# Kernel optimization log

Measured on AMD Instinct MI355X. Metric: run time of the kernel, lower is better.

The kernel has to match this reference:

```python
import jax, jax.numpy as jnp
import numpy as np

N_NODES = 50000
N_EDGES = 640000
DIM_IN = 128
DIM_OUT = 32
HEADS = 4
NEG_SLOPE = 0.2


def setup_inputs() -> dict:
    key = jax.random.key(0)
    ks = jax.random.split(key, 8)
    HC = HEADS * DIM_OUT
    x = jax.random.normal(ks[0], (N_NODES, DIM_IN), dtype=jnp.float32)
    edge_index = jax.random.randint(ks[1], (2, N_EDGES), 0, N_NODES, dtype=jnp.int32)
    s = 1.0 / np.sqrt(DIM_IN)
    Wl = jax.random.normal(ks[2], (DIM_IN, HC), dtype=jnp.float32) * s   # lin_l (source)
    Wr = jax.random.normal(ks[3], (DIM_IN, HC), dtype=jnp.float32) * s   # lin_r (target)
    att = jax.random.normal(ks[4], (HEADS, DIM_OUT), dtype=jnp.float32) * (1.0 / np.sqrt(DIM_OUT))
    bias = jnp.zeros((HC,), dtype=jnp.float32)
    Wp = jax.random.normal(ks[5], (HC, DIM_OUT), dtype=jnp.float32) * (1.0 / np.sqrt(HC))
    bp = jnp.zeros((DIM_OUT,), dtype=jnp.float32)
    return {"x": x, "edge_index": edge_index, "Wl": Wl, "Wr": Wr,
            "att": att, "bias": bias, "Wp": Wp, "bp": bp}


def reference(x, edge_index, Wl, Wr, att, bias, Wp, bp):
    N = x.shape[0]
    H, C = att.shape
    src = edge_index[0]  # j: message source
    dst = edge_index[1]  # i: message target (softmax segment)
    xl = (x @ Wl).reshape(N, H, C)  # source-side transform
    xr = (x @ Wr).reshape(N, H, C)  # target-side transform
    # GATv2: e_ij = a^T LeakyReLU(xl_j + xr_i)
    e = jax.nn.leaky_relu(xl[src] + xr[dst], NEG_SLOPE)        # [E,H,C]
    logits = jnp.einsum('ehc,hc->eh', e, att)                  # [E,H]
    m = jax.ops.segment_max(logits, dst, num_segments=N)       # [N,H]
    ex = jnp.exp(logits - m[dst])
    denom = jax.ops.segment_sum(ex, dst, num_segments=N)       # [N,H]
    alpha = ex / (denom[dst] + 1e-16)                          # [E,H]
    msg = xl[src] * alpha[:, :, None]                          # [E,H,C]
    out = jax.ops.segment_sum(msg, dst, num_segments=N)        # [N,H,C]
    out = out.reshape(N, H * C) + bias                         # concat heads + bias
    return out @ Wp + bp                                       # proj to dim_out
```

## Files before the change

kernel.cpp:

```cpp
#include <hip/hip_runtime.h>
#include <hip/hip_bf16.h>
#include <math.h>

#define N_NODES 50000
#define N_EDGES 640000
#define HEADS 4
#define CDIM 32
#define HC 128
#define DIN 128
#define DOUT 32
#define NEG_SLOPE 0.2f
#define TPAD 136
#define BCAP 64
#define NPB 16
#define EPT 4
#define ZERO_NB ((N_NODES + 255) / 256)
#define WT_NB (2 * DIN * HC / 256)
#define WPT_NB (DOUT * HC / 256)
#define FILL_NB (N_EDGES / (256 * EPT))
#define TF_NB ((N_NODES + 127) / 128)

typedef __hip_bfloat16 bf16;
typedef __attribute__((ext_vector_type(8))) short short8;
typedef __attribute__((ext_vector_type(4))) float floatx4;
typedef __attribute__((ext_vector_type(2))) float floatx2;
typedef __attribute__((ext_vector_type(4))) unsigned short ushort4v;

static __device__ __forceinline__ float bflo(unsigned w) { return __uint_as_float(w << 16); }
static __device__ __forceinline__ float bfhi(unsigned w) { return __uint_as_float(w & 0xFFFF0000u); }
static __device__ __forceinline__ unsigned short f2bf(float f) {
    union { bf16 h; unsigned short u; } cv; cv.h = __float2bfloat16(f); return cv.u;
}

__global__ __launch_bounds__(256) void k_prep(
    unsigned* __restrict__ cnt,
    const float* __restrict__ Wl, const float* __restrict__ Wr,
    const float* __restrict__ bias, const float* __restrict__ Wp,
    const float* __restrict__ bp,
    bf16* __restrict__ WlF, bf16* __restrict__ WrF, bf16* __restrict__ WpT,
    float* __restrict__ cvec)
{
    const int t = threadIdx.x, b = blockIdx.x;
    if (b < ZERO_NB) {
        const int i = b * 256 + t;
        if (i < N_NODES) cnt[i] = 0u;
    } else if (b < ZERO_NB + WT_NB) {
        const int i = (b - ZERO_NB) * 256 + t;
        const int i2 = (i < DIN * HC) ? i : i - DIN * HC;
        const int c = i2 >> 7, j = i2 & 127;
        const int jt = j >> 4, m = j & 15;
        const int kk = c >> 5, quad = (c >> 3) & 3, u = c & 7;
        const int idx = (jt * 4 + kk) * 512 + (quad * 16 + m) * 8 + u;
        if (i < DIN * HC) WlF[idx] = __float2bfloat16(Wl[i2]);
        else              WrF[idx] = __float2bfloat16(Wr[i2]);
    } else if (b < ZERO_NB + WT_NB + WPT_NB) {
        const int i = (b - ZERO_NB - WT_NB) * 256 + t;
        const int c = i >> 5, j = i & 31;
        WpT[j * HC + c] = __float2bfloat16(Wp[i]);
    } else {
        __shared__ float part[8][32];
        const int j = t & 31, ch = t >> 5;
        float v = 0.f;
        for (int c = ch * 16; c < ch * 16 + 16; c++)
            v += bias[c] * Wp[c * DOUT + j];
        part[ch][j] = v;
        __syncthreads();
        if (t < 32) {
            float s = bp[t];
            #pragma unroll
            for (int k = 0; k < 8; k++) s += part[k][t];
            cvec[t] = s;
        }
    }
}

__global__ __launch_bounds__(256) void k_fill_tf(
    const int* __restrict__ ei, unsigned* __restrict__ cnt,
    unsigned short* __restrict__ srcs,
    const float* __restrict__ x,
    const bf16* __restrict__ WlF, const bf16* __restrict__ WrF,
    bf16* __restrict__ xl, bf16* __restrict__ xr)
{
    const int t = threadIdx.x, b = blockIdx.x;

    if (b < FILL_NB) {
        const int e0 = (b * 256 + t) * EPT;
        const int4 sv = *(const int4*)(ei + e0);
        const int4 dv = *(const int4*)(ei + N_EDGES + e0);
        const int s[4] = {sv.x, sv.y, sv.z, sv.w};
        const int d[4] = {dv.x, dv.y, dv.z, dv.w};
        unsigned pos[4];
        #pragma unroll
        for (int i = 0; i < EPT; i++)
            pos[i] = atomicAdd(&cnt[d[i]], 1u);
        #pragma unroll
        for (int i = 0; i < EPT; i++)
            if (pos[i] < BCAP)
                srcs[((size_t)d[i] << 6) + pos[i]] = (unsigned short)s[i];
        return;
    }

    const int n0 = (b - FILL_NB) * 128;
    const int w = t >> 6, lane = t & 63;
    const int m = lane & 15, quad = lane >> 4;
    const int na = n0 + w * 32 + m;
    const int nb = na + 16;
    const bool va = (na < N_NODES), vb = (nb < N_NODES);

    const float* xpa = x + (size_t)(va ? na : 0) * DIN;
    const float* xpb = x + (size_t)(vb ? nb : 0) * DIN;
    short8 afa[4], afb[4];
    #pragma unroll
    for (int kk = 0; kk < 4; kk++) {
        const float4 la = *(const float4*)(xpa + kk * 32 + quad * 8);
        const float4 ha = *(const float4*)(xpa + kk * 32 + quad * 8 + 4);
        const float4 lb = *(const float4*)(xpb + kk * 32 + quad * 8);
        const float4 hb = *(const float4*)(xpb + kk * 32 + quad * 8 + 4);
        short8 va8, vb8;
        va8[0] = (short)f2bf(la.x); va8[1] = (short)f2bf(la.y);
        va8[2] = (short)f2bf(la.z); va8[3] = (short)f2bf(la.w);
        va8[4] = (short)f2bf(ha.x); va8[5] = (short)f2bf(ha.y);
        va8[6] = (short)f2bf(ha.z); va8[7] = (short)f2bf(ha.w);
        vb8[0] = (short)f2bf(lb.x); vb8[1] = (short)f2bf(lb.y);
        vb8[2] = (short)f2bf(lb.z); vb8[3] = (short)f2bf(lb.w);
        vb8[4] = (short)f2bf(hb.x); vb8[5] = (short)f2bf(hb.y);
        vb8[6] = (short)f2bf(hb.z); vb8[7] = (short)f2bf(hb.w);
        afa[kk] = va8;
        afb[kk] = vb8;
    }

    const short8* wlf = (const short8*)WlF;
    const short8* wrf = (const short8*)WrF;
    #pragma unroll
    for (int jt = 0; jt < 8; jt++) {
        floatx4 aLa = {0.f,0.f,0.f,0.f}, aLb = {0.f,0.f,0.f,0.f};
        floatx4 aRa = {0.f,0.f,0.f,0.f}, aRb = {0.f,0.f,0.f,0.f};
        #pragma unroll
        for (int kk = 0; kk < 4; kk++) {
            const short8 bl = wlf[(jt * 4 + kk) * 64 + lane];
            const short8 br = wrf[(jt * 4 + kk) * 64 + lane];
            aLa = __builtin_amdgcn_mfma_f32_16x16x32_bf16(bl, afa[kk], aLa, 0, 0, 0);
            aLb = __builtin_amdgcn_mfma_f32_16x16x32_bf16(bl, afb[kk], aLb, 0, 0, 0);
            aRa = __builtin_amdgcn_mfma_f32_16x16x32_bf16(br, afa[kk], aRa, 0, 0, 0);
            aRb = __builtin_amdgcn_mfma_f32_16x16x32_bf16(br, afb[kk], aRb, 0, 0, 0);
        }
        const int joff = jt * 16 + quad * 4;
        if (va) {
            ushort4v pl, pr;
            #pragma unroll
            for (int r = 0; r < 4; r++) { pl[r] = f2bf(aLa[r]); pr[r] = f2bf(aRa[r]); }
            *(ushort4v*)(xl + (size_t)na * HC + joff) = pl;
            *(ushort4v*)(xr + (size_t)na * HC + joff) = pr;
        }
        if (vb) {
            ushort4v pl, pr;
            #pragma unroll
            for (int r = 0; r < 4; r++) { pl[r] = f2bf(aLb[r]); pr[r] = f2bf(aRb[r]); }
            *(ushort4v*)(xl + (size_t)nb * HC + joff) = pl;
            *(ushort4v*)(xr + (size_t)nb * HC + joff) = pr;
        }
    }
}

static __device__ __forceinline__ uint4 gat(
    const int srcj, const int e, const int cn,
    const unsigned* __restrict__ xl2, const int hq)
{
    const int s = __shfl(srcj, e & 63, 64);
    const size_t row = (size_t)((e < cn) ? s : 0) << 6;
    return ((const uint4*)(xl2 + row))[hq];
}

static __device__ __forceinline__ void consume_edge(
    const uint4 bx, const int eidx, const int cn,
    const floatx2* __restrict__ xr2v, const floatx2* __restrict__ a2v,
    float& s_run, floatx2* __restrict__ acc2)
{
    floatx2 x2[4];
    x2[0] = floatx2{bflo(bx.x), bfhi(bx.x)};
    x2[1] = floatx2{bflo(bx.y), bfhi(bx.y)};
    x2[2] = floatx2{bflo(bx.z), bfhi(bx.z)};
    x2[3] = floatx2{bflo(bx.w), bfhi(bx.w)};
    floatx2 p2 = {0.f, 0.f};
    #pragma unroll
    for (int k = 0; k < 4; k++) {
        const floatx2 v = x2[k] + xr2v[k];
        const floatx2 vn = v * NEG_SLOPE;
        floatx2 lr;
        lr.x = fmaxf(v.x, vn.x);
        lr.y = fmaxf(v.y, vn.y);
        p2 += a2v[k] * lr;
    }
    float p = p2.x + p2.y;
    p += __shfl_xor(p, 1, 64);
    p += __shfl_xor(p, 2, 64);
    const float e_ = (eidx < cn) ? __expf(p) : 0.f;
    s_run += e_;
    #pragma unroll
    for (int k = 0; k < 4; k++) acc2[k] += x2[k] * e_;
}

__global__ __launch_bounds__(256) void k_agg(
    const unsigned short* __restrict__ srcs, const unsigned* __restrict__ cnt,
    const unsigned* __restrict__ xl2,
    const unsigned* __restrict__ xr2,
    const float* __restrict__ att,
    const bf16* __restrict__ WpT,
    const float* __restrict__ cvec,
    float* __restrict__ out)
{
    __shared__ __align__(16) unsigned short srow[NPB][TPAD];
    const int t = threadIdx.x;
    const int w = t >> 6, lane = t & 63;
    const int es = lane >> 4, hq = lane & 15;

    const float4 av0 = ((const float4*)att)[hq * 2];
    const float4 av1 = ((const float4*)att)[hq * 2 + 1];
    floatx2 a2[4];
    a2[0] = floatx2{av0.x, av0.y}; a2[1] = floatx2{av0.z, av0.w};
    a2[2] = floatx2{av1.x, av1.y}; a2[3] = floatx2{av1.z, av1.w};

    const int nb0 = blockIdx.x * NPB + w * 4;
    const uint4 cv4 = *(const uint4*)(cnt + nb0);
    int cns[4];
    cns[0] = (int)(cv4.x < 64u ? cv4.x : 64u);
    cns[1] = (int)(cv4.y < 64u ? cv4.y : 64u);
    cns[2] = (int)(cv4.z < 64u ? cv4.z : 64u);
    cns[3] = (int)(cv4.w < 64u ? cv4.w : 64u);
    int srcjv[4];
    uint4 xru[4];
    #pragma unroll
    for (int ni = 0; ni < 4; ni++) {
        srcjv[ni] = (int)srcs[((size_t)(nb0 + ni) << 6) + lane];
        xru[ni] = ((const uint4*)(xr2 + (size_t)(nb0 + ni) * 64))[hq];
    }

    #pragma unroll
    for (int ni = 0; ni < 4; ni++) {
        const int cn = cns[ni];
        floatx2 xr2v[4];
        xr2v[0] = floatx2{bflo(xru[ni].x), bfhi(xru[ni].x)};
        xr2v[1] = floatx2{bflo(xru[ni].y), bfhi(xru[ni].y)};
        xr2v[2] = floatx2{bflo(xru[ni].z), bfhi(xru[ni].z)};
        xr2v[3] = floatx2{bflo(xru[ni].w), bfhi(xru[ni].w)};
        float s_run = 0.f;
        floatx2 acc2[4];
        acc2[0] = floatx2{0.f, 0.f}; acc2[1] = floatx2{0.f, 0.f};
        acc2[2] = floatx2{0.f, 0.f}; acc2[3] = floatx2{0.f, 0.f};
        const int sj = srcjv[ni];

        uint4 b0 = gat(sj, es,      cn, xl2, hq);
        uint4 b1 = gat(sj, es + 4,  cn, xl2, hq);
        uint4 b2 = gat(sj, es + 8,  cn, xl2, hq);
        uint4 b3 = gat(sj, es + 12, cn, xl2, hq);
        for (int i = 0; i < cn; i += 16) {
            const bool more = (i + 16 < cn);
            consume_edge(b0, i + es,      cn, xr2v, a2, s_run, acc2);
            if (more) b0 = gat(sj, i + 16 + es, cn, xl2, hq);
            consume_edge(b1, i + es + 4,  cn, xr2v, a2, s_run, acc2);
            if (more) b1 = gat(sj, i + 20 + es, cn, xl2, hq);
            consume_edge(b2, i + es + 8,  cn, xr2v, a2, s_run, acc2);
            if (more) b2 = gat(sj, i + 24 + es, cn, xl2, hq);
            consume_edge(b3, i + es + 12, cn, xr2v, a2, s_run, acc2);
            if (more) b3 = gat(sj, i + 28 + es, cn, xl2, hq);
        }
        s_run += __shfl_xor(s_run, 16, 64);
        s_run += __shfl_xor(s_run, 32, 64);
        #pragma unroll
        for (int k = 0; k < 4; k++) {
            acc2[k].x += __shfl_xor(acc2[k].x, 16, 64);
            acc2[k].x += __shfl_xor(acc2[k].x, 32, 64);
            acc2[k].y += __shfl_xor(acc2[k].y, 16, 64);
            acc2[k].y += __shfl_xor(acc2[k].y, 32, 64);
        }
        const float rden = 1.f / (s_run + 1e-16f);

        if (es == 0) {
            union { unsigned short s[8]; uint4 v; } pk;
            #pragma unroll
            for (int k = 0; k < 4; k++) {
                pk.s[2 * k]     = f2bf(acc2[k].x * rden);
                pk.s[2 * k + 1] = f2bf(acc2[k].y * rden);
            }
            *(uint4*)&srow[w * 4 + ni][hq * 8] = pk.v;
        }
    }
    __syncthreads();

    if (w < 2) {
        const int m = lane & 15, quad = lane >> 4;
        short8 af[4];
        #pragma unroll
        for (int kk = 0; kk < 4; kk++)
            af[kk] = *(const short8*)&srow[m][kk * 32 + quad * 8];
        floatx4 d = {0.f, 0.f, 0.f, 0.f};
        #pragma unroll
        for (int kk = 0; kk < 4; kk++) {
            const short8 bfr = *(const short8*)(WpT + (w * 16 + m) * HC + kk * 32 + quad * 8);
            d = __builtin_amdgcn_mfma_f32_16x16x32_bf16(af[kk], bfr, d, 0, 0, 0);
        }
        const int jj = w * 16 + m;
        const float cv = cvec[jj];
        #pragma unroll
        for (int r = 0; r < 4; r++) {
            const int node = blockIdx.x * NPB + quad * 4 + r;
            out[(size_t)node * DOUT + jj] = d[r] + cv;
        }
    }
}

extern "C" void kernel_launch(void* const* d_in, const int* in_sizes, int n_in,
                              void* d_out, int out_size, void* d_ws, size_t ws_size,
                              hipStream_t stream)
{
    const float* x    = (const float*)d_in[0];
    const int*   ei   = (const int*)d_in[1];
    const float* Wl   = (const float*)d_in[2];
    const float* Wr   = (const float*)d_in[3];
    const float* att  = (const float*)d_in[4];
    const float* bias = (const float*)d_in[5];
    const float* Wp   = (const float*)d_in[6];
    const float* bp   = (const float*)d_in[7];
    float* out = (float*)d_out;

    bf16* xl       = (bf16*)d_ws;
    bf16* xr       = xl + (size_t)N_NODES * HC;
    bf16* WlF      = xr + (size_t)N_NODES * HC;
    bf16* WrF      = WlF + DIN * HC;
    bf16* WpT      = WrF + DIN * HC;
    float* cvec    = (float*)(WpT + DOUT * HC);
    unsigned* cnt  = (unsigned*)(cvec + DOUT);
    unsigned short* srcs = (unsigned short*)(cnt + N_NODES);

    k_prep<<<ZERO_NB + WT_NB + WPT_NB + 1, 256, 0, stream>>>(
        cnt, Wl, Wr, bias, Wp, bp, WlF, WrF, WpT, cvec);
    k_fill_tf<<<FILL_NB + TF_NB, 256, 0, stream>>>(ei, cnt, srcs, x,
                                                   WlF, WrF, xl, xr);
    k_agg<<<N_NODES / NPB, 256, 0, stream>>>(srcs, cnt,
        (const unsigned*)xl, (const unsigned*)xr, att, WpT, cvec, out);
}
```

Measured before the change: 167.0 us.

## Fuse prep and fill/transform kernels with an atomic readiness flag

Merges the weight-prep kernel into the edge-fill/transform kernel. Transform blocks spin on a global ready counter until the prep blocks have published the bf16 weights. The counter zeroing moves to a hipMemsetAsync, which removes one kernel launch and its boundary. The cost is a spin-wait that depends on prep blocks being scheduled first, plus an extra memset launch.

After: 233.7 us. 1.4x slower.

```diff
diff --git a/kernel.cpp b/kernel.cpp
--- a/kernel.cpp
+++ b/kernel.cpp
@@ -14,11 +14,12 @@
 #define BCAP 64
 #define NPB 16
 #define EPT 4
-#define ZERO_NB ((N_NODES + 255) / 256)
 #define WT_NB (2 * DIN * HC / 256)
 #define WPT_NB (DOUT * HC / 256)
+#define PREP2 (WT_NB + WPT_NB + 1)
 #define FILL_NB (N_EDGES / (256 * EPT))
 #define TF_NB ((N_NODES + 127) / 128)
+#define GRID1 (PREP2 + FILL_NB + TF_NB)
 
 typedef __hip_bfloat16 bf16;
 typedef __attribute__((ext_vector_type(8))) short short8;
@@ -32,59 +33,56 @@
     union { bf16 h; unsigned short u; } cv; cv.h = __float2bfloat16(f); return cv.u;
 }
 
-__global__ __launch_bounds__(256) void k_prep(
-    unsigned* __restrict__ cnt,
+__global__ __launch_bounds__(256) void k_fused(
+    const int* __restrict__ ei, const float* __restrict__ x,
     const float* __restrict__ Wl, const float* __restrict__ Wr,
     const float* __restrict__ bias, const float* __restrict__ Wp,
     const float* __restrict__ bp,
+    unsigned* __restrict__ cnt, unsigned* __restrict__ ready,
+    unsigned short* __restrict__ srcs,
     bf16* __restrict__ WlF, bf16* __restrict__ WrF, bf16* __restrict__ WpT,
-    float* __restrict__ cvec)
-{
+    float* __restrict__ cvec,
+    bf16* __restrict__ xl, bf16* __restrict__ xr)
+{
+    __shared__ float part[8][32];
     const int t = threadIdx.x, b = blockIdx.x;
-    if (b < ZERO_NB) {
-        const int i = b * 256 + t;
-        if (i < N_NODES) cnt[i] = 0u;
-    } else if (b < ZERO_NB + WT_NB) {
-        const int i = (b - ZERO_NB) * 256 + t;
-        const int i2 = (i < DIN * HC) ? i : i - DIN * HC;
-        const int c = i2 >> 7, j = i2 & 127;
-        const int jt = j >> 4, m = j & 15;
-        const int kk = c >> 5, quad = (c >> 3) & 3, u = c & 7;
-        const int idx = (jt * 4 + kk) * 512 + (quad * 16 + m) * 8 + u;
-        if (i < DIN * HC) WlF[idx] = __float2bfloat16(Wl[i2]);
-        else              WrF[idx] = __float2bfloat16(Wr[i2]);
-    } else if (b < ZERO_NB + WT_NB + WPT_NB) {
-        const int i = (b - ZERO_NB - WT_NB) * 256 + t;
-        const int c = i >> 5, j = i & 31;
-        WpT[j * HC + c] = __float2bfloat16(Wp[i]);
-    } else {
-        __shared__ float part[8][32];
-        const int j = t & 31, ch = t >> 5;
-        float v = 0.f;
-        for (int c = ch * 16; c < ch * 16 + 16; c++)
-            v += bias[c] * Wp[c * DOUT + j];
-        part[ch][j] = v;
+
+    if (b < PREP2) {
+        if (b < WT_NB) {
+            const int i = b * 256 + t;
+            const int i2 = (i < DIN * HC) ? i : i - DIN * HC;
+            const int c = i2 >> 7, j = i2 & 127;
+            const int jt = j >> 4, m = j & 15;
+            const int kk = c >> 5, quad = (c >> 3) & 3, u = c & 7;
+            const int idx = (jt * 4 + kk) * 512 + (quad * 16 + m) * 8 + u;
+            if (i < DIN * HC) WlF[idx] = __float2bfloat16(Wl[i2]);
+            else              WrF[idx] = __float2bfloat16(Wr[i2]);
+        } else if (b < WT_NB + WPT_NB) {
+            const int i = (b - WT_NB) * 256 + t;
+            const int c = i >> 5, j = i & 31;
+            WpT[j * HC + c] = __float2bfloat16(Wp[i]);
+        } else {
+            const int j = t & 31, ch = t >> 5;
+            float v = 0.f;
+            for (int c = ch * 16; c < ch * 16 + 16; c++)
+                v += bias[c] * Wp[c * DOUT + j];
+            part[ch][j] = v;
+            __syncthreads();
+            if (t < 32) {
+                float s = bp[t];
+                #pragma unroll
+                for (int k = 0; k < 8; k++) s += part[k][t];
+                cvec[t] = s;
+            }
+        }
+        __threadfence();
         __syncthreads();
-        if (t < 32) {
-            float s = bp[t];
-            #pragma unroll
-            for (int k = 0; k < 8; k++) s += part[k][t];
-            cvec[t] = s;
-        }
-    }
-}
-
-__global__ __launch_bounds__(256) void k_fill_tf(
-    const int* __restrict__ ei, unsigned* __restrict__ cnt,
-    unsigned short* __restrict__ srcs,
-    const float* __restrict__ x,
-    const bf16* __restrict__ WlF, const bf16* __restrict__ WrF,
-    bf16* __restrict__ xl, bf16* __restrict__ xr)
-{
-    const int t = threadIdx.x, b = blockIdx.x;
-
-    if (b < FILL_NB) {
-        const int e0 = (b * 256 + t) * EPT;
+        if (t == 0) atomicAdd(ready, 1u);
+        return;
+    }
+
+    if (b < PREP2 + FILL_NB) {
+        const int e0 = ((b - PREP2) * 256 + t) * EPT;
         const int4 sv = *(const int4*)(ei + e0);
         const int4 dv = *(const int4*)(ei + N_EDGES + e0);
         const int s[4] = {sv.x, sv.y, sv.z, sv.w};
@@ -100,7 +98,15 @@
         return;
     }
 
-    const int n0 = (b - FILL_NB) * 128;
+    if (t == 0) {
+        while (__hip_atomic_load(ready, __ATOMIC_ACQUIRE,
+                                 __HIP_MEMORY_SCOPE_AGENT) < (unsigned)PREP2)
+            __builtin_amdgcn_s_sleep(2);
+    }
+    __syncthreads();
+    __threadfence();
+
+    const int n0 = (b - PREP2 - FILL_NB) * 128;
     const int w = t >> 6, lane = t & 63;
     const int m = lane & 15, quad = lane >> 4;
     const int na = n0 + w * 32 + m;
@@ -330,12 +336,14 @@
     bf16* WpT      = WrF + DIN * HC;
     float* cvec    = (float*)(WpT + DOUT * HC);
     unsigned* cnt  = (unsigned*)(cvec + DOUT);
-    unsigned short* srcs = (unsigned short*)(cnt + N_NODES);
-
-    k_prep<<<ZERO_NB + WT_NB + WPT_NB + 1, 256, 0, stream>>>(
-        cnt, Wl, Wr, bias, Wp, bp, WlF, WrF, WpT, cvec);
-    k_fill_tf<<<FILL_NB + TF_NB, 256, 0, stream>>>(ei, cnt, srcs, x,
-                                                   WlF, WrF, xl, xr);
+    unsigned* ready = cnt + N_NODES;
+    unsigned short* srcs = (unsigned short*)(cnt + N_NODES + 8);
+
+    hipMemsetAsync(cnt, 0, (N_NODES + 8) * sizeof(unsigned), stream);
+
+    k_fused<<<GRID1, 256, 0, stream>>>(ei, x, Wl, Wr, bias, Wp, bp,
+                                       cnt, ready, srcs,
+                                       WlF, WrF, WpT, cvec, xl, xr);
     k_agg<<<N_NODES / NPB, 256, 0, stream>>>(srcs, cnt,
         (const unsigned*)xl, (const unsigned*)xr, att, WpT, cvec, out);
 }
```
